# Optimization experiments

Measured on AMD Instinct MI355X. Metric: run time of the kernel, lower is better.

## Reference

```python
import jax, jax.numpy as jnp
import numpy as np

# ---- hash-grid config (from module source) ----
L = 16          # n_levels
F = 2           # n_features_per_level
T = 1 << 19     # hashmap size
BASE = 16
SCALE = 1.3819
RES = [int(np.floor(BASE * SCALE ** l)) for l in range(L)]
DENSE = [(r + 1) ** 3 <= T for r in RES]   # levels 0-4 dense, rest hashed
PRIMES = np.array([1, 2654435761, 805459861], dtype=np.uint32)
OFFS = np.array([[i, j, k] for k in (0, 1) for j in (0, 1) for i in (0, 1)], dtype=np.float32)  # [8,3]
OFFS_U = OFFS.astype(np.uint32)


def hash_grid_encode(xyz, table):
    # xyz: [N,3] in [0,1); table: [L,T,F]
    feats = []
    for l in range(L):
        res = RES[l]
        pos = xyz * res                      # [N,3]
        p0f = jnp.floor(pos)
        w = pos - p0f                        # trilinear weights, [N,3]
        p0 = p0f.astype(jnp.uint32)          # [N,3]
        corner = p0[:, None, :] + OFFS_U[None]            # [N,8,3] uint32
        if DENSE[l]:
            s = np.uint32(res + 1)
            idx = corner[..., 0] + corner[..., 1] * s + corner[..., 2] * (s * s)
        else:
            idx = (corner[..., 0] * PRIMES[0]) ^ (corner[..., 1] * PRIMES[1]) ^ (corner[..., 2] * PRIMES[2])
            idx = idx % np.uint32(T)
        # corner weights: prod_d (offs ? w : 1-w)  -> [N,8]
        wts = jnp.prod(jnp.where(OFFS[None].astype(bool), w[:, None, :], 1.0 - w[:, None, :]), axis=-1)
        f = table[l][idx]                    # gather: [N,8,F]
        feats.append(jnp.sum(f * wts[..., None], axis=1))  # [N,F]
    return jnp.concatenate(feats, axis=-1)   # [N, L*F=32]


def sh_deg4(d):
    # d in [-1,1]^3; returns [N,16] real SH basis (tcnn ordering/constants)
    x, y, z = d[:, 0], d[:, 1], d[:, 2]
    x2, y2, z2 = x * x, y * y, z * z
    xy, yz, xz = x * y, y * z, x * z
    return jnp.stack([
        jnp.full_like(x, 0.28209479177387814),
        -0.48860251190291987 * y,
        0.48860251190291987 * z,
        -0.48860251190291987 * x,
        1.0925484305920792 * xy,
        -1.0925484305920792 * yz,
        0.94617469575755997 * z2 - 0.31539156525251999,
        -1.0925484305920792 * xz,
        0.54627421529603959 * (x2 - y2),
        0.59004358992664352 * y * (-3.0 * x2 + y2),
        2.8906114426405538 * xy * z,
        0.45704579946446572 * y * (1.0 - 5.0 * z2),
        0.3731763325901154 * z * (5.0 * z2 - 3.0),
        0.45704579946446572 * x * (1.0 - 5.0 * z2),
        1.4453057213202769 * z * (x2 - y2),
        0.59004358992664352 * x * (-x2 + 3.0 * y2),
    ], axis=-1)


def setup_inputs() -> dict:
    key = jax.random.key(0)
    ks = jax.random.split(key, 8)
    N = 2 ** 21
    xyz = jax.random.uniform(ks[0], (N, 3), dtype=jnp.float32)
    dir = jax.random.uniform(ks[1], (N, 3), dtype=jnp.float32)
    # hash table init per tcnn: uniform in [-1e-4, 1e-4]
    hash_table = jax.random.uniform(ks[2], (L, T, F), dtype=jnp.float32, minval=-1e-4, maxval=1e-4)
    def he(k, fan_in, shape):
        return jax.random.normal(k, shape, dtype=jnp.float32) * np.sqrt(2.0 / fan_in)
    w_sigma1 = he(ks[3], 32, (32, 64))
    w_sigma2 = he(ks[4], 64, (64, 17))   # 1 + geo_feat_dim(16)
    w_rgb1 = he(ks[5], 32, (32, 64))     # 16 (SH) + 16 (geo)
    w_rgb2 = he(ks[6], 64, (64, 64))
    w_rgb3 = he(ks[7], 64, (64, 3))
    return {"xyz": xyz, "dir": dir, "hash_table": hash_table,
            "w_sigma1": w_sigma1, "w_sigma2": w_sigma2,
            "w_rgb1": w_rgb1, "w_rgb2": w_rgb2, "w_rgb3": w_rgb3}


def reference(xyz, dir, hash_table, w_sigma1, w_sigma2, w_rgb1, w_rgb2, w_rgb3):
    xyz_flat = xyz.reshape(-1, 3)
    dir_flat = dir.reshape(-1, 3)
    enc = hash_grid_encode(xyz_flat, hash_table)                 # [N,32]
    h = jax.nn.relu(enc @ w_sigma1)
    geometry = h @ w_sigma2                                       # [N,17]
    sigma, geo_feat = geometry[..., :1], geometry[..., 1:]
    dir_enc = sh_deg4(dir_flat * 2.0 - 1.0)                       # [N,16]
    rgb_in = jnp.concatenate([dir_enc, geo_feat], axis=-1)        # [N,32]
    h = jax.nn.relu(rgb_in @ w_rgb1)
    h = jax.nn.relu(h @ w_rgb2)
    rgb = h @ w_rgb3                                              # [N,3]
    rgb_unflat = rgb.reshape(xyz.shape)
    sigma_unflat = sigma.reshape(xyz.shape[:-1] + (1,))
    return jax.nn.sigmoid(rgb_unflat), jax.nn.relu(sigma_unflat)
```

## Files before the change

### kernel.cpp

```cpp
#include <hip/hip_runtime.h>
#include <hip/hip_bf16.h>
#include <cmath>

#define TBL (1 << 19)

__device__ __forceinline__ float relu_f(float x) { return fmaxf(x, 0.0f); }

__device__ __forceinline__ unsigned short f2bf(float x) {
    union { float f; unsigned u; } v; v.f = x;
    const unsigned r = v.u + 0x7FFFu + ((v.u >> 16) & 1u);
    return (unsigned short)(r >> 16);
}

typedef __attribute__((ext_vector_type(8))) short short8;
typedef __attribute__((ext_vector_type(4))) float floatx4;

#define RES_LIST {16, 22, 30, 42, 58, 80, 111, 153, 212, 294, 406, 561, 775, 1072, 1481, 2047}

__global__ __launch_bounds__(256, 8)
void encode_pinned(const float* __restrict__ xyz,
                   const float* __restrict__ table,
                   float* __restrict__ ws_enc,
                   unsigned levels_packed,
                   int n)
{
    constexpr unsigned RES[16] = RES_LIST;

    const unsigned sub = blockIdx.x & 7u;
    const unsigned level = (levels_packed >> (4u * sub)) & 0xFu;
    const int i = (int)(blockIdx.x >> 3) * 256 + (int)threadIdx.x;
    if (i >= n) return;

    const float px_ = __builtin_nontemporal_load(xyz + 3 * (size_t)i + 0);
    const float py_ = __builtin_nontemporal_load(xyz + 3 * (size_t)i + 1);
    const float pz_ = __builtin_nontemporal_load(xyz + 3 * (size_t)i + 2);

    const unsigned res = RES[level];
    const float fr = (float)res;
    const float posx = px_ * fr, posy = py_ * fr, posz = pz_ * fr;
    const float fx = floorf(posx), fy = floorf(posy), fz = floorf(posz);
    const float wx = posx - fx, wy = posy - fy, wz = posz - fz;
    const unsigned x0 = (unsigned)fx, y0 = (unsigned)fy, z0 = (unsigned)fz;
    const float* tb = table + (size_t)level * (TBL * 2);

    float a0 = 0.0f, a1 = 0.0f;
    if (level < 5) {
        const unsigned s = res + 1u;
        const unsigned s2 = s * s;
#pragma unroll
        for (int c = 0; c < 8; ++c) {
            const unsigned cx = x0 + (c & 1);
            const unsigned cy = y0 + ((c >> 1) & 1);
            const unsigned cz = z0 + ((c >> 2) & 1);
            const unsigned idx = cx + cy * s + cz * s2;
            const float w = ((c & 1) ? wx : 1.0f - wx) *
                            ((c & 2) ? wy : 1.0f - wy) *
                            ((c & 4) ? wz : 1.0f - wz);
            const float2 f = *reinterpret_cast<const float2*>(tb + 2u * idx);
            a0 = fmaf(f.x, w, a0);
            a1 = fmaf(f.y, w, a1);
        }
    } else {
#pragma unroll
        for (int c = 0; c < 8; ++c) {
            const unsigned cx = x0 + (c & 1);
            const unsigned cy = y0 + ((c >> 1) & 1);
            const unsigned cz = z0 + ((c >> 2) & 1);
            unsigned idx = (cx * 1u) ^ (cy * 2654435761u) ^ (cz * 805459861u);
            idx &= (unsigned)(TBL - 1);
            const float w = ((c & 1) ? wx : 1.0f - wx) *
                            ((c & 2) ? wy : 1.0f - wy) *
                            ((c & 4) ? wz : 1.0f - wz);
            const float2 f = *reinterpret_cast<const float2*>(tb + 2u * idx);
            a0 = fmaf(f.x, w, a0);
            a1 = fmaf(f.y, w, a1);
        }
    }

    float* dst = ws_enc + 2 * ((size_t)level * n + i);
    __builtin_nontemporal_store(a0, dst + 0);
    __builtin_nontemporal_store(a1, dst + 1);
}

__global__ __launch_bounds__(256)
void mlp_mfma(const float* __restrict__ ws_enc,
              const float* __restrict__ dirv,
              const float* __restrict__ ws1,
              const float* __restrict__ ws2,
              const float* __restrict__ wr1,
              const float* __restrict__ wr2,
              const float* __restrict__ wr3,
              float* __restrict__ out,
              int n)
{
    __shared__ alignas(16) unsigned short s_w[13184];
    __shared__ alignas(16) unsigned short s_act[4 * 16 * 72];
    __shared__ alignas(16) float          s_geo[4 * 16 * 20];

    const int tid = threadIdx.x;

    for (int e = tid; e < 13184; e += 256) s_w[e] = 0;
    __syncthreads();
    for (int e = tid; e < 2048; e += 256) { const int k = e >> 6, j = e & 63; s_w[0     + j * 40 + k] = f2bf(ws1[e]); }
    for (int e = tid; e < 1088; e += 256) { const int k = e / 17, j = e % 17; s_w[2560  + j * 72 + k] = f2bf(ws2[e]); }
    for (int e = tid; e < 2048; e += 256) { const int k = e >> 6, j = e & 63; s_w[4864  + j * 40 + k] = f2bf(wr1[e]); }
    for (int e = tid; e < 4096; e += 256) { const int k = e >> 6, j = e & 63; s_w[7424  + j * 72 + k] = f2bf(wr2[e]); }
    for (int e = tid; e < 192;  e += 256) { const int k = e / 3,  j = e % 3;  s_w[12032 + j * 72 + k] = f2bf(wr3[e]); }
    __syncthreads();

    const int wave = tid >> 6;
    const int lane = tid & 63;
    const int q    = lane >> 4;
    const int mr   = lane & 15;
    unsigned short* hb = s_act + wave * (16 * 72);
    float*          gb = s_geo + wave * (16 * 20);
    const int base = blockIdx.x * 256 + wave * 64;
    if (base >= n) return;

#pragma unroll 1
    for (int mt = 0; mt < 4; ++mt) {
        const int pt = base + mt * 16 + mr;

        short8 aenc;
#pragma unroll
        for (int t = 0; t < 4; ++t) {
            const float2 e = *reinterpret_cast<const float2*>(ws_enc + 2 * ((size_t)(q * 4 + t) * n + pt));
            aenc[2 * t + 0] = (short)f2bf(e.x);
            aenc[2 * t + 1] = (short)f2bf(e.y);
        }

#pragma unroll
        for (int nc = 0; nc < 4; ++nc) {
            const short8 b = *reinterpret_cast<const short8*>(s_w + 0 + (nc * 16 + mr) * 40 + q * 8);
            floatx4 acc = {0.f, 0.f, 0.f, 0.f};
            acc = __builtin_amdgcn_mfma_f32_16x16x32_bf16(aenc, b, acc, 0, 0, 0);
#pragma unroll
            for (int r = 0; r < 4; ++r)
                hb[(q * 4 + r) * 72 + nc * 16 + mr] = f2bf(fmaxf(acc[r], 0.f));
        }
        __builtin_amdgcn_wave_barrier();

        {
            const short8 a0 = *reinterpret_cast<const short8*>(hb + mr * 72 + 0  + q * 8);
            const short8 a1 = *reinterpret_cast<const short8*>(hb + mr * 72 + 32 + q * 8);
            floatx4 acc0 = {0.f, 0.f, 0.f, 0.f};
            floatx4 acc1 = {0.f, 0.f, 0.f, 0.f};
            {
                const short8 b0 = *reinterpret_cast<const short8*>(s_w + 2560 + mr * 72 + 0  + q * 8);
                const short8 b1 = *reinterpret_cast<const short8*>(s_w + 2560 + mr * 72 + 32 + q * 8);
                acc0 = __builtin_amdgcn_mfma_f32_16x16x32_bf16(a0, b0, acc0, 0, 0, 0);
                acc0 = __builtin_amdgcn_mfma_f32_16x16x32_bf16(a1, b1, acc0, 0, 0, 0);
            }
            {
                const short8 b0 = *reinterpret_cast<const short8*>(s_w + 2560 + (16 + mr) * 72 + 0  + q * 8);
                const short8 b1 = *reinterpret_cast<const short8*>(s_w + 2560 + (16 + mr) * 72 + 32 + q * 8);
                acc1 = __builtin_amdgcn_mfma_f32_16x16x32_bf16(a0, b0, acc1, 0, 0, 0);
                acc1 = __builtin_amdgcn_mfma_f32_16x16x32_bf16(a1, b1, acc1, 0, 0, 0);
            }
#pragma unroll
            for (int r = 0; r < 4; ++r) gb[(q * 4 + r) * 20 + mr + 3] = acc0[r];
            if (mr == 0) {
#pragma unroll
                for (int r = 0; r < 4; ++r) gb[(q * 4 + r) * 20 + 19] = acc1[r];
            }
        }
        __builtin_amdgcn_wave_barrier();

        if (lane < 16)
            out[3 * (size_t)n + (size_t)(base + mt * 16 + lane)] = fmaxf(gb[lane * 20 + 3], 0.f);

        const float dx = dirv[3 * (size_t)pt + 0] * 2.0f - 1.0f;
        const float dy = dirv[3 * (size_t)pt + 1] * 2.0f - 1.0f;
        const float dz = dirv[3 * (size_t)pt + 2] * 2.0f - 1.0f;
        const float x2 = dx * dx, y2 = dy * dy, z2 = dz * dz;
        const float xy = dx * dy, yz = dy * dz, xz = dx * dz;
        float sh[16];
        sh[0]  = 0.28209479177387814f;
        sh[1]  = -0.48860251190291987f * dy;
        sh[2]  = 0.48860251190291987f * dz;
        sh[3]  = -0.48860251190291987f * dx;
        sh[4]  = 1.0925484305920792f * xy;
        sh[5]  = -1.0925484305920792f * yz;
        sh[6]  = 0.94617469575756f * z2 - 0.31539156525252f;
        sh[7]  = -1.0925484305920792f * xz;
        sh[8]  = 0.5462742152960396f * (x2 - y2);
        sh[9]  = 0.5900435899266435f * dy * (-3.0f * x2 + y2);
        sh[10] = 2.890611442640554f * xy * dz;
        sh[11] = 0.4570457994644657f * dy * (1.0f - 5.0f * z2);
        sh[12] = 0.3731763325901154f * dz * (5.0f * z2 - 3.0f);
        sh[13] = 0.4570457994644657f * dx * (1.0f - 5.0f * z2);
        sh[14] = 1.445305721320277f * dz * (x2 - y2);
        sh[15] = 0.5900435899266435f * dx * (-x2 + 3.0f * y2);

        short8 ar;
        if (q < 2) {
#pragma unroll
            for (int j = 0; j < 8; ++j) ar[j] = (short)f2bf(sh[q * 8 + j]);
        } else {
            const floatx4 g0 = *reinterpret_cast<const floatx4*>(gb + mr * 20 + 4 + (q - 2) * 8);
            const floatx4 g1 = *reinterpret_cast<const floatx4*>(gb + mr * 20 + 8 + (q - 2) * 8);
#pragma unroll
            for (int j = 0; j < 4; ++j) { ar[j] = (short)f2bf(g0[j]); ar[4 + j] = (short)f2bf(g1[j]); }
        }

#pragma unroll
        for (int nc = 0; nc < 4; ++nc) {
            const short8 b = *reinterpret_cast<const short8*>(s_w + 4864 + (nc * 16 + mr) * 40 + q * 8);
            floatx4 acc = {0.f, 0.f, 0.f, 0.f};
            acc = __builtin_amdgcn_mfma_f32_16x16x32_bf16(ar, b, acc, 0, 0, 0);
#pragma unroll
            for (int r = 0; r < 4; ++r)
                hb[(q * 4 + r) * 72 + nc * 16 + mr] = f2bf(fmaxf(acc[r], 0.f));
        }
        __builtin_amdgcn_wave_barrier();

        {
            const short8 a0 = *reinterpret_cast<const short8*>(hb + mr * 72 + 0  + q * 8);
            const short8 a1 = *reinterpret_cast<const short8*>(hb + mr * 72 + 32 + q * 8);
            __builtin_amdgcn_wave_barrier();
#pragma unroll
            for (int nc = 0; nc < 4; ++nc) {
                const short8 b0 = *reinterpret_cast<const short8*>(s_w + 7424 + (nc * 16 + mr) * 72 + 0  + q * 8);
                const short8 b1 = *reinterpret_cast<const short8*>(s_w + 7424 + (nc * 16 + mr) * 72 + 32 + q * 8);
                floatx4 acc = {0.f, 0.f, 0.f, 0.f};
                acc = __builtin_amdgcn_mfma_f32_16x16x32_bf16(a0, b0, acc, 0, 0, 0);
                acc = __builtin_amdgcn_mfma_f32_16x16x32_bf16(a1, b1, acc, 0, 0, 0);
#pragma unroll
                for (int r = 0; r < 4; ++r)
                    hb[(q * 4 + r) * 72 + nc * 16 + mr] = f2bf(fmaxf(acc[r], 0.f));
            }
        }
        __builtin_amdgcn_wave_barrier();

        {
            const short8 a0 = *reinterpret_cast<const short8*>(hb + mr * 72 + 0  + q * 8);
            const short8 a1 = *reinterpret_cast<const short8*>(hb + mr * 72 + 32 + q * 8);
            const short8 b0 = *reinterpret_cast<const short8*>(s_w + 12032 + mr * 72 + 0  + q * 8);
            const short8 b1 = *reinterpret_cast<const short8*>(s_w + 12032 + mr * 72 + 32 + q * 8);
            floatx4 acc = {0.f, 0.f, 0.f, 0.f};
            acc = __builtin_amdgcn_mfma_f32_16x16x32_bf16(a0, b0, acc, 0, 0, 0);
            acc = __builtin_amdgcn_mfma_f32_16x16x32_bf16(a1, b1, acc, 0, 0, 0);
            if (mr < 3) {
#pragma unroll
                for (int r = 0; r < 4; ++r) {
                    const int p = base + mt * 16 + q * 4 + r;
                    out[3 * (size_t)p + mr] = 1.0f / (1.0f + __expf(-acc[r]));
                }
            }
        }
        __builtin_amdgcn_wave_barrier();
    }
}

__global__ __launch_bounds__(256, 4)
void nerf_fused(const float* __restrict__ xyz,
                const float* __restrict__ dirv,
                const float* __restrict__ table,
                const float* __restrict__ ws1,
                const float* __restrict__ ws2,
                const float* __restrict__ wr1,
                const float* __restrict__ wr2,
                const float* __restrict__ wr3,
                float* __restrict__ out,
                int n)
{
    constexpr unsigned RES[16] = RES_LIST;

    const int i = blockIdx.x * 256 + threadIdx.x;
    if (i >= n) return;

    const float px_ = xyz[3 * (size_t)i + 0];
    const float py_ = xyz[3 * (size_t)i + 1];
    const float pz_ = xyz[3 * (size_t)i + 2];

    float enc[32];
#pragma unroll
    for (int l = 0; l < 16; ++l) {
        const unsigned res = RES[l];
        const float fr = (float)res;
        const float posx = px_ * fr, posy = py_ * fr, posz = pz_ * fr;
        const float fx = floorf(posx), fy = floorf(posy), fz = floorf(posz);
        const float wx = posx - fx, wy = posy - fy, wz = posz - fz;
        const unsigned x0 = (unsigned)fx, y0 = (unsigned)fy, z0 = (unsigned)fz;
        const float* tb = table + (size_t)l * (TBL * 2);
        float a0 = 0.0f, a1 = 0.0f;
#pragma unroll
        for (int c = 0; c < 8; ++c) {
            const unsigned cx = x0 + (c & 1);
            const unsigned cy = y0 + ((c >> 1) & 1);
            const unsigned cz = z0 + ((c >> 2) & 1);
            unsigned idx;
            if (l < 5) {
                const unsigned s = res + 1u;
                idx = cx + cy * s + cz * (s * s);
            } else {
                idx = (cx * 1u) ^ (cy * 2654435761u) ^ (cz * 805459861u);
                idx &= (unsigned)(TBL - 1);
            }
            const float w = ((c & 1) ? wx : 1.0f - wx) *
                            ((c & 2) ? wy : 1.0f - wy) *
                            ((c & 4) ? wz : 1.0f - wz);
            const float2 f = *reinterpret_cast<const float2*>(tb + 2u * idx);
            a0 = fmaf(f.x, w, a0);
            a1 = fmaf(f.y, w, a1);
        }
        enc[2 * l + 0] = a0;
        enc[2 * l + 1] = a1;
    }

    float h[64];
#pragma unroll
    for (int j = 0; j < 64; ++j) h[j] = 0.0f;
#pragma unroll
    for (int k = 0; k < 32; ++k) {
        const float e = enc[k];
#pragma unroll
        for (int j = 0; j < 64; ++j) h[j] = fmaf(e, ws1[k * 64 + j], h[j]);
    }
#pragma unroll
    for (int j = 0; j < 64; ++j) h[j] = relu_f(h[j]);

    float geo[17];
#pragma unroll
    for (int j = 0; j < 17; ++j) geo[j] = 0.0f;
#pragma unroll
    for (int k = 0; k < 64; ++k) {
        const float e = h[k];
#pragma unroll
        for (int j = 0; j < 17; ++j) geo[j] = fmaf(e, ws2[k * 17 + j], geo[j]);
    }
    out[3 * (size_t)n + (size_t)i] = relu_f(geo[0]);

    const float dx = dirv[3 * (size_t)i + 0] * 2.0f - 1.0f;
    const float dy = dirv[3 * (size_t)i + 1] * 2.0f - 1.0f;
    const float dz = dirv[3 * (size_t)i + 2] * 2.0f - 1.0f;
    const float x2 = dx * dx, y2 = dy * dy, z2 = dz * dz;
    const float xy = dx * dy, yz = dy * dz, xz = dx * dz;

    float sh[16];
    sh[0]  = 0.28209479177387814f;
    sh[1]  = -0.48860251190291987f * dy;
    sh[2]  = 0.48860251190291987f * dz;
    sh[3]  = -0.48860251190291987f * dx;
    sh[4]  = 1.0925484305920792f * xy;
    sh[5]  = -1.0925484305920792f * yz;
    sh[6]  = 0.94617469575756f * z2 - 0.31539156525252f;
    sh[7]  = -1.0925484305920792f * xz;
    sh[8]  = 0.5462742152960396f * (x2 - y2);
    sh[9]  = 0.5900435899266435f * dy * (-3.0f * x2 + y2);
    sh[10] = 2.890611442640554f * xy * dz;
    sh[11] = 0.4570457994644657f * dy * (1.0f - 5.0f * z2);
    sh[12] = 0.3731763325901154f * dz * (5.0f * z2 - 3.0f);
    sh[13] = 0.4570457994644657f * dx * (1.0f - 5.0f * z2);
    sh[14] = 1.445305721320277f * dz * (x2 - y2);
    sh[15] = 0.5900435899266435f * dx * (-x2 + 3.0f * y2);

    float g[64];
#pragma unroll
    for (int j = 0; j < 64; ++j) g[j] = 0.0f;
#pragma unroll
    for (int k = 0; k < 16; ++k) {
        const float e = sh[k];
#pragma unroll
        for (int j = 0; j < 64; ++j) g[j] = fmaf(e, wr1[k * 64 + j], g[j]);
    }
#pragma unroll
    for (int k = 16; k < 32; ++k) {
        const float e = geo[k - 15];
#pragma unroll
        for (int j = 0; j < 64; ++j) g[j] = fmaf(e, wr1[k * 64 + j], g[j]);
    }
#pragma unroll
    for (int j = 0; j < 64; ++j) g[j] = relu_f(g[j]);

    float r0 = 0.0f, r1 = 0.0f, r2 = 0.0f;
#pragma unroll
    for (int half = 0; half < 2; ++half) {
        const int j0 = half * 32;
        float g2h[32];
#pragma unroll
        for (int j = 0; j < 32; ++j) g2h[j] = 0.0f;
#pragma unroll
        for (int k = 0; k < 64; ++k) {
            const float e = g[k];
#pragma unroll
            for (int j = 0; j < 32; ++j) g2h[j] = fmaf(e, wr2[k * 64 + j0 + j], g2h[j]);
        }
#pragma unroll
        for (int j = 0; j < 32; ++j) {
            const float e = relu_f(g2h[j]);
            r0 = fmaf(e, wr3[(j0 + j) * 3 + 0], r0);
            r1 = fmaf(e, wr3[(j0 + j) * 3 + 1], r1);
            r2 = fmaf(e, wr3[(j0 + j) * 3 + 2], r2);
        }
    }

    out[3 * (size_t)i + 0] = 1.0f / (1.0f + __expf(-r0));
    out[3 * (size_t)i + 1] = 1.0f / (1.0f + __expf(-r1));
    out[3 * (size_t)i + 2] = 1.0f / (1.0f + __expf(-r2));
}

extern "C" void kernel_launch(void* const* d_in, const int* in_sizes, int n_in,
                              void* d_out, int out_size, void* d_ws, size_t ws_size,
                              hipStream_t stream)
{
    const float* xyz   = (const float*)d_in[0];
    const float* dirv  = (const float*)d_in[1];
    const float* table = (const float*)d_in[2];
    const float* ws1   = (const float*)d_in[3];
    const float* ws2   = (const float*)d_in[4];
    const float* wr1   = (const float*)d_in[5];
    const float* wr2   = (const float*)d_in[6];
    const float* wr3   = (const float*)d_in[7];
    float* out = (float*)d_out;

    const int n = in_sizes[0] / 3;
    const int blocks_per_level = (n + 255) / 256;
    dim3 block(256);
    dim3 grid_mlp(blocks_per_level);
    dim3 grid_enc(8 * blocks_per_level);

    const size_t enc_bytes = (size_t)n * 16 * sizeof(float2);
    if (ws_size >= enc_bytes && (n & 255) == 0) {
        float* ws_enc = (float*)d_ws;
        hipLaunchKernelGGL(encode_pinned, grid_enc, block, 0, stream,
                           xyz, table, ws_enc, 0xCBA98765u, n);
        hipLaunchKernelGGL(encode_pinned, grid_enc, block, 0, stream,
                           xyz, table, ws_enc, 0x43210FEDu, n);
        hipLaunchKernelGGL(mlp_mfma, grid_mlp, block, 0, stream,
                           ws_enc, dirv, ws1, ws2, wr1, wr2, wr3, out, n);
    } else {
        hipLaunchKernelGGL(nerf_fused, grid_mlp, block, 0, stream,
                           xyz, dirv, table, ws1, ws2, wr1, wr2, wr3, out, n);
    }
}
```

Baseline: 1.107 ms.

## Merge encode launches with XCD-aware level/quarter schedule and paired x-corner loads

Replaces the two per-half-level encode launches with one launch that uses packed lookup tables to assign (level, point-quarter) work units to each XCD. The aim is to balance the heavier hashed levels across XCDs and keep each level's table slice resident in that XCD's L2. The corner loop now pairs the two x-neighbours. Dense levels load adjacent float2 entries, and hashed levels with even x0 fetch both corners in one aligned float4, since x0^h and (x0+1)^h differ only in the low bit. The new path requires n to be a multiple of 1024, and the schedule tables are hand-tuned for the 8-XCD layout.

```diff
diff --git a/kernel.cpp b/kernel.cpp
--- a/kernel.cpp
+++ b/kernel.cpp
@@ -18,17 +18,25 @@
 #define RES_LIST {16, 22, 30, 42, 58, 80, 111, 153, 212, 294, 406, 561, 775, 1072, 1481, 2047}
 
 __global__ __launch_bounds__(256, 8)
-void encode_pinned(const float* __restrict__ xyz,
-                   const float* __restrict__ table,
-                   float* __restrict__ ws_enc,
-                   unsigned levels_packed,
-                   int n)
+void encode_sched(const float* __restrict__ xyz,
+                  const float* __restrict__ table,
+                  float* __restrict__ ws_enc,
+                  int n)
 {
     constexpr unsigned RES[16] = RES_LIST;
-
-    const unsigned sub = blockIdx.x & 7u;
-    const unsigned level = (levels_packed >> (4u * sub)) & 0xFu;
-    const int i = (int)(blockIdx.x >> 3) * 256 + (int)threadIdx.x;
+    constexpr unsigned LEVP[8] = {0x00665555u, 0x00777766u, 0x11998888u, 0x11AAAA99u,
+                                  0x222CBBBBu, 0x332DDCCCu, 0x433EEEDDu, 0x444FFFFEu};
+    constexpr unsigned QTRP[8] = {0x44E4u, 0xEE4Eu, 0x44E4u, 0xEE4Eu,
+                                  0x90E4u, 0x4D39u, 0x3A4Eu, 0xE793u};
+
+    const int xcd      = (int)(blockIdx.x & 7u);
+    const unsigned g   = blockIdx.x >> 3;
+    const unsigned upb = (unsigned)(n >> 10);
+    const int unit     = (int)(g / upb);
+    const int slot     = (int)(g % upb);
+    const int level    = (int)((LEVP[xcd] >> (4 * unit)) & 15u);
+    const int quarter  = (int)((QTRP[xcd] >> (2 * unit)) & 3u);
+    const int i        = quarter * (n >> 2) + slot * 256 + (int)threadIdx.x;
     if (i >= n) return;
 
     const float px_ = __builtin_nontemporal_load(xyz + 3 * (size_t)i + 0);
@@ -44,36 +52,45 @@
     const float* tb = table + (size_t)level * (TBL * 2);
 
     float a0 = 0.0f, a1 = 0.0f;
+    const float wx1 = wx, wx0 = 1.0f - wx;
+
     if (level < 5) {
         const unsigned s = res + 1u;
         const unsigned s2 = s * s;
-#pragma unroll
-        for (int c = 0; c < 8; ++c) {
-            const unsigned cx = x0 + (c & 1);
-            const unsigned cy = y0 + ((c >> 1) & 1);
-            const unsigned cz = z0 + ((c >> 2) & 1);
-            const unsigned idx = cx + cy * s + cz * s2;
-            const float w = ((c & 1) ? wx : 1.0f - wx) *
-                            ((c & 2) ? wy : 1.0f - wy) *
-                            ((c & 4) ? wz : 1.0f - wz);
-            const float2 f = *reinterpret_cast<const float2*>(tb + 2u * idx);
-            a0 = fmaf(f.x, w, a0);
-            a1 = fmaf(f.y, w, a1);
+        const unsigned base = x0 + y0 * s + z0 * s2;
+#pragma unroll
+        for (int c = 0; c < 4; ++c) {
+            const unsigned dy = c & 1, dz = c >> 1;
+            const unsigned idx = base + dy * s + dz * s2;
+            const float wyz = (dy ? wy : 1.0f - wy) * (dz ? wz : 1.0f - wz);
+            const float w0 = wyz * wx0, w1 = wyz * wx1;
+            const float2 f0 = *reinterpret_cast<const float2*>(tb + 2u * idx);
+            const float2 f1 = *reinterpret_cast<const float2*>(tb + 2u * idx + 2u);
+            a0 = fmaf(f0.x, w0, fmaf(f1.x, w1, a0));
+            a1 = fmaf(f0.y, w0, fmaf(f1.y, w1, a1));
         }
     } else {
 #pragma unroll
-        for (int c = 0; c < 8; ++c) {
-            const unsigned cx = x0 + (c & 1);
-            const unsigned cy = y0 + ((c >> 1) & 1);
-            const unsigned cz = z0 + ((c >> 2) & 1);
-            unsigned idx = (cx * 1u) ^ (cy * 2654435761u) ^ (cz * 805459861u);
-            idx &= (unsigned)(TBL - 1);
-            const float w = ((c & 1) ? wx : 1.0f - wx) *
-                            ((c & 2) ? wy : 1.0f - wy) *
-                            ((c & 4) ? wz : 1.0f - wz);
-            const float2 f = *reinterpret_cast<const float2*>(tb + 2u * idx);
-            a0 = fmaf(f.x, w, a0);
-            a1 = fmaf(f.y, w, a1);
+        for (int c = 0; c < 4; ++c) {
+            const unsigned dy = c & 1, dz = c >> 1;
+            const unsigned hh = (y0 + dy) * 2654435761u ^ (z0 + dz) * 805459861u;
+            const float wyz = (dy ? wy : 1.0f - wy) * (dz ? wz : 1.0f - wz);
+            const float w0 = wyz * wx0, w1 = wyz * wx1;
+            const unsigned i0 = (x0 ^ hh) & (unsigned)(TBL - 1);
+            if (!(x0 & 1u)) {
+                const float4 f = *reinterpret_cast<const float4*>(tb + 2u * (i0 & ~1u));
+                const bool hi = (i0 & 1u) != 0u;
+                const float e0x = hi ? f.z : f.x, e0y = hi ? f.w : f.y;
+                const float e1x = hi ? f.x : f.z, e1y = hi ? f.y : f.w;
+                a0 = fmaf(e0x, w0, fmaf(e1x, w1, a0));
+                a1 = fmaf(e0y, w0, fmaf(e1y, w1, a1));
+            } else {
+                const unsigned i1 = ((x0 + 1u) ^ hh) & (unsigned)(TBL - 1);
+                const float2 f0 = *reinterpret_cast<const float2*>(tb + 2u * i0);
+                const float2 f1 = *reinterpret_cast<const float2*>(tb + 2u * i1);
+                a0 = fmaf(f0.x, w0, fmaf(f1.x, w1, a0));
+                a1 = fmaf(f0.y, w0, fmaf(f1.y, w1, a1));
+            }
         }
     }
 
@@ -418,15 +435,13 @@
     const int blocks_per_level = (n + 255) / 256;
     dim3 block(256);
     dim3 grid_mlp(blocks_per_level);
-    dim3 grid_enc(8 * blocks_per_level);
 
     const size_t enc_bytes = (size_t)n * 16 * sizeof(float2);
-    if (ws_size >= enc_bytes && (n & 255) == 0) {
+    if (ws_size >= enc_bytes && n >= 1024 && (n & 1023) == 0) {
         float* ws_enc = (float*)d_ws;
-        hipLaunchKernelGGL(encode_pinned, grid_enc, block, 0, stream,
-                           xyz, table, ws_enc, 0xCBA98765u, n);
-        hipLaunchKernelGGL(encode_pinned, grid_enc, block, 0, stream,
-                           xyz, table, ws_enc, 0x43210FEDu, n);
+        dim3 grid_enc(8u * 8u * (unsigned)(n >> 10));
+        hipLaunchKernelGGL(encode_sched, grid_enc, block, 0, stream,
+                           xyz, table, ws_enc, n);
         hipLaunchKernelGGL(mlp_mfma, grid_mlp, block, 0, stream,
                            ws_enc, dirv, ws1, ws2, wr1, wr2, wr3, out, n);
     } else {
```

Result: faster. 1.050 ms (-5.2%).
